# Kernel tuning notes

Measured on AMD Instinct MI355X. Metric: run time of the kernel, lower is better.

Reference implementation:

```python
import jax, jax.numpy as jnp
import numpy as np

EPS = 1e-08


def _center(K):
    # H K H with H = I - 11^T/n, expressed as O(n^2) double mean-subtraction
    rm = K.mean(axis=-1, keepdims=True)
    cm = K.mean(axis=-2, keepdims=True)
    tm = K.mean(axis=(-1, -2), keepdims=True)
    return K - rm - cm + tm


def setup_inputs() -> dict:
    key = jax.random.key(0)
    k1, k2 = jax.random.split(key)
    L, B, n, d = 5, 8, 1024, 64
    teacher = jax.random.normal(k1, (L, B, n, d), dtype=jnp.float32)
    student = jax.random.normal(k2, (L, B, n, d), dtype=jnp.float32)
    return {"teacher": teacher, "student": student}


def reference(teacher, student):
    # teacher, student: [L, B, n, d]  (internal=True, dim>=3 branch)
    cX = _center(jnp.einsum('lbnd,lbmd->lbnm', teacher, teacher))  # [L,B,n,n]
    cY = _center(jnp.einsum('lbnd,lbmd->lbnm', student, student))  # [L,B,n,n]
    hsic_xy = jnp.sum(cX * cY, axis=(-1, -2))  # [L,B]
    var_x = jnp.sqrt(jnp.sum(cX * cX, axis=(-1, -2)))  # [L,B]
    var_y = jnp.sqrt(jnp.sum(cY * cY, axis=(-1, -2)))  # [L,B]
    ratio = jnp.abs(hsic_xy / (var_x * var_y))  # [L,B]
    loss_per_layer = -jnp.log(ratio.mean(axis=-1) + EPS)  # [L]
    return loss_per_layer.mean()  # sum over layers / length
```

## Files before the change

kernel.cpp:

```cpp
#include <hip/hip_runtime.h>
#include <math.h>

#define LL 5
#define BB 8
#define NN 1024
#define DD 64
#define LB 40
#define SPLIT 16
#define KC (NN / SPLIT)
#define ZC (2 * DD)
#define NQ 3

#define GP_SHORTS (LB * SPLIT * NQ * 4096)
#define GP_FLOATS (GP_SHORTS / 2)
#define SP_OFF GP_FLOATS
#define ACC_OFF (GP_FLOATS + LB * SPLIT * ZC)

typedef short short8 __attribute__((ext_vector_type(8)));
typedef float floatx4 __attribute__((ext_vector_type(4)));

__device__ __forceinline__ unsigned short f2bf(float f) {
    union { float f; unsigned u; } v; v.f = f;
    const unsigned u = v.u;
    return (unsigned short)((u + 0x7FFFu + ((u >> 16) & 1u)) >> 16);
}
__device__ __forceinline__ float bf2f(unsigned short h) {
    union { unsigned u; float f; } v; v.u = ((unsigned)h) << 16; return v.f;
}
__device__ __forceinline__ float bflo(unsigned u) {
    union { unsigned u; float f; } v; v.u = u << 16; return v.f;
}
__device__ __forceinline__ float bfhi(unsigned u) {
    union { unsigned u; float f; } v; v.u = u & 0xFFFF0000u; return v.f;
}

__device__ __forceinline__ short8 read_frag(const short* Zt, int tbase, int lane, int k0) {
    const int c = tbase + (lane & 15);
    const int o = (k0 >> 3) + (lane >> 4);
    const int oct = (o ^ ((c + (c >> 4)) & 15)) & 7;
    return *(const short8*)(Zt + c * 64 + (oct << 3));
}

__global__ __launch_bounds__(256) void gram_kernel(const float* __restrict__ X,
                                                   const float* __restrict__ Y,
                                                   unsigned* __restrict__ Gp,
                                                   float* __restrict__ Sp) {
    __shared__ short Zt[ZC * KC];
    __shared__ float cscr[8][ZC];

    const int lb = blockIdx.y, nc = blockIdx.x, tid = threadIdx.x;
    const int r0 = nc * KC;
    const float4* X4 = (const float4*)(X + (size_t)lb * NN * DD);
    const float4* Y4 = (const float4*)(Y + (size_t)lb * NN * DD);

    const int col4 = tid & 31;
    const int rb = tid >> 5;
    float4 v[8];
#pragma unroll
    for (int m = 0; m < 8; ++m) {
        const int row = 8 * rb + m;
        v[m] = (col4 < 16) ? X4[(size_t)(r0 + row) * 16 + col4]
                           : Y4[(size_t)(r0 + row) * 16 + (col4 - 16)];
    }

#pragma unroll
    for (int e = 0; e < 4; ++e) {
        const int c = 4 * col4 + e;
        short8 w8;
        float cs = 0.f;
#pragma unroll
        for (int m = 0; m < 8; ++m) {
            const float fv = (e == 0) ? v[m].x : (e == 1) ? v[m].y : (e == 2) ? v[m].z : v[m].w;
            const unsigned short b = f2bf(fv);
            cs += bf2f(b);
            w8[m] = (short)b;
        }
        const int oct = (rb ^ ((c + (c >> 4)) & 15)) & 7;
        *(short8*)(Zt + c * 64 + (oct << 3)) = w8;
        cscr[rb][c] = cs;
    }
    __syncthreads();
    if (tid < ZC) {
        float s = 0.f;
#pragma unroll
        for (int g = 0; g < 8; ++g) s += cscr[g][tid];
        Sp[(lb * SPLIT + nc) * ZC + tid] = s;
    }

    const int lane = tid & 63, w = tid >> 6;
    const int jbeg = (w < 2) ? 0 : 4;

    floatx4 acc[2][8];
#pragma unroll
    for (int i = 0; i < 2; ++i)
#pragma unroll
        for (int j = 0; j < 8; ++j) acc[i][j] = (floatx4){0.f, 0.f, 0.f, 0.f};

#pragma unroll
    for (int k0 = 0; k0 < KC; k0 += 32) {
        short8 af[2], bfr[8];
#pragma unroll
        for (int i = 0; i < 2; ++i) af[i] = read_frag(Zt, (2 * w + i) * 16, lane, k0);
#pragma unroll
        for (int j = 0; j < 8; ++j)
            if (j >= jbeg) bfr[j] = read_frag(Zt, j * 16, lane, k0);
#pragma unroll
        for (int i = 0; i < 2; ++i)
#pragma unroll
            for (int j = 0; j < 8; ++j)
                if (j >= jbeg)
                    acc[i][j] = __builtin_amdgcn_mfma_f32_16x16x32_bf16(af[i], bfr[j], acc[i][j], 0, 0, 0);
    }

    unsigned* Gb = Gp + (size_t)(lb * SPLIT + nc) * (NQ * 2048);
    const int g = lane >> 4, cl = lane & 15;
#pragma unroll
    for (int i = 0; i < 2; ++i)
#pragma unroll
        for (int j = 0; j < 8; ++j) {
            if (j < jbeg) continue;
            const int slab = (w < 2) ? ((j < 4) ? 0 : 1) : 2;
            const int qrow0 = (w < 2 ? (2 * w + i) : (2 * (w - 2) + i)) * 16 + g * 4;
            const int qcol = (j & 3) * 16 + cl;
            if (w < 2 || j >= 4) {
                const unsigned lo = (unsigned)f2bf(acc[i][j][0]) | ((unsigned)f2bf(acc[i][j][1]) << 16);
                const unsigned hi = (unsigned)f2bf(acc[i][j][2]) | ((unsigned)f2bf(acc[i][j][3]) << 16);
                Gb[slab * 2048 + (qrow0 >> 1) * 64 + qcol] = lo;
                Gb[slab * 2048 + ((qrow0 >> 1) + 1) * 64 + qcol] = hi;
            }
        }
}

__global__ __launch_bounds__(256) void reduce_kernel(const unsigned* __restrict__ Gp,
                                                     const float* __restrict__ Sp,
                                                     float* __restrict__ Acc2) {
    const int b = blockIdx.x;
    const int lb = b / (NQ * 4);
    const int rem = b % (NQ * 4);
    const int q = rem >> 2, seg = rem & 3;
    const int tid = threadIdx.x;

    __shared__ float stot[ZC];
    __shared__ float red[4];

    if (tid < ZC) {
        float s = 0.f;
#pragma unroll
        for (int sp = 0; sp < SPLIT; ++sp) s += Sp[(lb * SPLIT + sp) * ZC + tid];
        stot[tid] = s;
    }
    __syncthreads();

    const int u0 = seg * 512 + tid * 2;
    const int rp = u0 >> 6;
    const int c0 = u0 & 63;

    float g00 = 0.f, g10 = 0.f, g01 = 0.f, g11 = 0.f;
#pragma unroll
    for (int sp = 0; sp < SPLIT; ++sp) {
        const uint2 p = *(const uint2*)&Gp[((size_t)(lb * SPLIT + sp) * NQ + q) * 2048 + u0];
        g00 += bflo(p.x); g10 += bfhi(p.x);
        g01 += bflo(p.y); g11 += bfhi(p.y);
    }
    const int rowbase = (q == 2) ? 64 : 0;
    const int colbase = (q == 0) ? 0 : 64;
    const float inv_n = 1.0f / (float)NN;
    const float sr0 = stot[rowbase + 2 * rp] * inv_n;
    const float sr1 = stot[rowbase + 2 * rp + 1] * inv_n;
    const float sc0 = stot[colbase + c0];
    const float sc1 = stot[colbase + c0 + 1];
    float sq = 0.f;
    { const float cv = g00 - sr0 * sc0; sq += cv * cv; }
    { const float cv = g10 - sr1 * sc0; sq += cv * cv; }
    { const float cv = g01 - sr0 * sc1; sq += cv * cv; }
    { const float cv = g11 - sr1 * sc1; sq += cv * cv; }

#pragma unroll
    for (int off = 32; off; off >>= 1) sq += __shfl_down(sq, off);
    const int wave = tid >> 6;
    if ((tid & 63) == 0) red[wave] = sq;
    __syncthreads();
    if (tid == 0)
        Acc2[lb * 12 + q * 4 + seg] = red[0] + red[1] + red[2] + red[3];
}

__global__ void final_kernel(const float* __restrict__ Acc2, float* __restrict__ out) {
    const int tid = threadIdx.x;
    float v = 0.0f;
    if (tid < LB) {
        float vxx = 0.f, hxy = 0.f, vyy = 0.f;
#pragma unroll
        for (int s = 0; s < 4; ++s) {
            vxx += Acc2[tid * 12 + s];
            hxy += Acc2[tid * 12 + 4 + s];
            vyy += Acc2[tid * 12 + 8 + s];
        }
        v = fabsf(hxy / (sqrtf(vxx) * sqrtf(vyy)));
    }
    v += __shfl_xor(v, 1);
    v += __shfl_xor(v, 2);
    v += __shfl_xor(v, 4);
    float loss = 0.0f;
#pragma unroll
    for (int l = 0; l < LL; ++l) {
        const float sl = __shfl(v, l * BB);
        loss += -logf(sl * (1.0f / (float)BB) + 1e-8f);
    }
    if (tid == 0) out[0] = loss * (1.0f / (float)LL);
}

extern "C" void kernel_launch(void* const* d_in, const int* in_sizes, int n_in,
                              void* d_out, int out_size, void* d_ws, size_t ws_size,
                              hipStream_t stream) {
    const float* teacher = (const float*)d_in[0];
    const float* student = (const float*)d_in[1];
    float* ws = (float*)d_ws;
    unsigned* Gp = (unsigned*)ws;
    float* Sp = ws + SP_OFF;
    float* Acc2 = ws + ACC_OFF;

    dim3 grid1(SPLIT, LB);
    gram_kernel<<<grid1, 256, 0, stream>>>(teacher, student, Gp, Sp);
    reduce_kernel<<<LB * NQ * 4, 256, 0, stream>>>(Gp, Sp, Acc2);
    final_kernel<<<1, 64, 0, stream>>>(Acc2, (float*)d_out);
}
```

Baseline: 77.30 us.

## Fuse gram, reduce and final kernels via atomic last-block election

Merges the three kernel launches into one kernel. Each lb's last-arriving split block, detected with an atomic counter, reduces that lb's partial Gram slabs, and the last lb block computes the final loss. This removes two launch boundaries and their gaps, at the cost of serialising each lb's reduction onto a single block (12x less parallelism for that stage) and adding a memset launch for the counters.

```diff
diff --git a/kernel.cpp b/kernel.cpp
--- a/kernel.cpp
+++ b/kernel.cpp
@@ -14,7 +14,8 @@
 #define GP_SHORTS (LB * SPLIT * NQ * 4096)
 #define GP_FLOATS (GP_SHORTS / 2)
 #define SP_OFF GP_FLOATS
-#define ACC_OFF (GP_FLOATS + LB * SPLIT * ZC)
+#define ACC_OFF (SP_OFF + LB * SPLIT * ZC)
+#define CNT_OFF (ACC_OFF + LB * 4)
 
 typedef short short8 __attribute__((ext_vector_type(8)));
 typedef float floatx4 __attribute__((ext_vector_type(4)));
@@ -41,107 +42,114 @@
     return *(const short8*)(Zt + c * 64 + (oct << 3));
 }
 
-__global__ __launch_bounds__(256) void gram_kernel(const float* __restrict__ X,
-                                                   const float* __restrict__ Y,
-                                                   unsigned* __restrict__ Gp,
-                                                   float* __restrict__ Sp) {
+__global__ __launch_bounds__(256) void cka_all(const float* __restrict__ X,
+                                               const float* __restrict__ Y,
+                                               unsigned* __restrict__ Gp,
+                                               float* __restrict__ Sp,
+                                               float* __restrict__ Acc,
+                                               unsigned* __restrict__ cnt,
+                                               float* __restrict__ out) {
     __shared__ short Zt[ZC * KC];
     __shared__ float cscr[8][ZC];
-
-    const int lb = blockIdx.y, nc = blockIdx.x, tid = threadIdx.x;
-    const int r0 = nc * KC;
-    const float4* X4 = (const float4*)(X + (size_t)lb * NN * DD);
-    const float4* Y4 = (const float4*)(Y + (size_t)lb * NN * DD);
-
-    const int col4 = tid & 31;
-    const int rb = tid >> 5;
-    float4 v[8];
-#pragma unroll
-    for (int m = 0; m < 8; ++m) {
-        const int row = 8 * rb + m;
-        v[m] = (col4 < 16) ? X4[(size_t)(r0 + row) * 16 + col4]
-                           : Y4[(size_t)(r0 + row) * 16 + (col4 - 16)];
-    }
-
-#pragma unroll
-    for (int e = 0; e < 4; ++e) {
-        const int c = 4 * col4 + e;
-        short8 w8;
-        float cs = 0.f;
+    __shared__ float stot[ZC];
+    __shared__ float redq[NQ][4];
+    __shared__ int elect;
+
+    const int bid = blockIdx.x;
+    const int tid = threadIdx.x;
+    const int lb = bid / SPLIT, nc = bid % SPLIT;
+
+    {
+        const int r0 = nc * KC;
+        const float4* X4 = (const float4*)(X + (size_t)lb * NN * DD);
+        const float4* Y4 = (const float4*)(Y + (size_t)lb * NN * DD);
+
+        const int col4 = tid & 31;
+        const int rb = tid >> 5;
+        float4 v[8];
 #pragma unroll
         for (int m = 0; m < 8; ++m) {
-            const float fv = (e == 0) ? v[m].x : (e == 1) ? v[m].y : (e == 2) ? v[m].z : v[m].w;
-            const unsigned short b = f2bf(fv);
-            cs += bf2f(b);
-            w8[m] = (short)b;
-        }
-        const int oct = (rb ^ ((c + (c >> 4)) & 15)) & 7;
-        *(short8*)(Zt + c * 64 + (oct << 3)) = w8;
-        cscr[rb][c] = cs;
-    }
-    __syncthreads();
-    if (tid < ZC) {
-        float s = 0.f;
-#pragma unroll
-        for (int g = 0; g < 8; ++g) s += cscr[g][tid];
-        Sp[(lb * SPLIT + nc) * ZC + tid] = s;
-    }
-
-    const int lane = tid & 63, w = tid >> 6;
-    const int jbeg = (w < 2) ? 0 : 4;
-
-    floatx4 acc[2][8];
-#pragma unroll
-    for (int i = 0; i < 2; ++i)
-#pragma unroll
-        for (int j = 0; j < 8; ++j) acc[i][j] = (floatx4){0.f, 0.f, 0.f, 0.f};
-
-#pragma unroll
-    for (int k0 = 0; k0 < KC; k0 += 32) {
-        short8 af[2], bfr[8];
-#pragma unroll
-        for (int i = 0; i < 2; ++i) af[i] = read_frag(Zt, (2 * w + i) * 16, lane, k0);
-#pragma unroll
-        for (int j = 0; j < 8; ++j)
-            if (j >= jbeg) bfr[j] = read_frag(Zt, j * 16, lane, k0);
+            const int row = 8 * rb + m;
+            v[m] = (col4 < 16) ? X4[(size_t)(r0 + row) * 16 + col4]
+                               : Y4[(size_t)(r0 + row) * 16 + (col4 - 16)];
+        }
+
+#pragma unroll
+        for (int e = 0; e < 4; ++e) {
+            const int c = 4 * col4 + e;
+            short8 w8;
+            float cs = 0.f;
+#pragma unroll
+            for (int m = 0; m < 8; ++m) {
+                const float fv = (e == 0) ? v[m].x : (e == 1) ? v[m].y
+                               : (e == 2) ? v[m].z : v[m].w;
+                const unsigned short b = f2bf(fv);
+                cs += bf2f(b);
+                w8[m] = (short)b;
+            }
+            const int oct = (rb ^ ((c + (c >> 4)) & 15)) & 7;
+            *(short8*)(Zt + c * 64 + (oct << 3)) = w8;
+            cscr[rb][c] = cs;
+        }
+        __syncthreads();
+        if (tid < ZC) {
+            float s = 0.f;
+#pragma unroll
+            for (int g = 0; g < 8; ++g) s += cscr[g][tid];
+            Sp[(lb * SPLIT + nc) * ZC + tid] = s;
+        }
+
+        const int lane = tid & 63, w = tid >> 6;
+        const int jbeg = (w < 2) ? 0 : 4;
+
+        floatx4 acc[2][8];
 #pragma unroll
         for (int i = 0; i < 2; ++i)
 #pragma unroll
+            for (int j = 0; j < 8; ++j) acc[i][j] = (floatx4){0.f, 0.f, 0.f, 0.f};
+
+#pragma unroll
+        for (int k0 = 0; k0 < KC; k0 += 32) {
+            short8 af[2], bfr[8];
+#pragma unroll
+            for (int i = 0; i < 2; ++i) af[i] = read_frag(Zt, (2 * w + i) * 16, lane, k0);
+#pragma unroll
             for (int j = 0; j < 8; ++j)
-                if (j >= jbeg)
-                    acc[i][j] = __builtin_amdgcn_mfma_f32_16x16x32_bf16(af[i], bfr[j], acc[i][j], 0, 0, 0);
-    }
-
-    unsigned* Gb = Gp + (size_t)(lb * SPLIT + nc) * (NQ * 2048);
-    const int g = lane >> 4, cl = lane & 15;
-#pragma unroll
-    for (int i = 0; i < 2; ++i)
-#pragma unroll
-        for (int j = 0; j < 8; ++j) {
-            if (j < jbeg) continue;
-            const int slab = (w < 2) ? ((j < 4) ? 0 : 1) : 2;
-            const int qrow0 = (w < 2 ? (2 * w + i) : (2 * (w - 2) + i)) * 16 + g * 4;
-            const int qcol = (j & 3) * 16 + cl;
-            if (w < 2 || j >= 4) {
+                if (j >= jbeg) bfr[j] = read_frag(Zt, j * 16, lane, k0);
+#pragma unroll
+            for (int i = 0; i < 2; ++i)
+#pragma unroll
+                for (int j = 0; j < 8; ++j)
+                    if (j >= jbeg)
+                        acc[i][j] = __builtin_amdgcn_mfma_f32_16x16x32_bf16(af[i], bfr[j], acc[i][j], 0, 0, 0);
+        }
+
+        unsigned* Gb = Gp + (size_t)(lb * SPLIT + nc) * (NQ * 2048);
+        const int g = lane >> 4, cl = lane & 15;
+#pragma unroll
+        for (int i = 0; i < 2; ++i)
+#pragma unroll
+            for (int j = 0; j < 8; ++j) {
+                if (j < jbeg) continue;
+                const int slab = (w < 2) ? ((j < 4) ? 0 : 1) : 2;
+                const int qrow0 = (w < 2 ? (2 * w + i) : (2 * (w - 2) + i)) * 16 + g * 4;
+                const int qcol = (j & 3) * 16 + cl;
                 const unsigned lo = (unsigned)f2bf(acc[i][j][0]) | ((unsigned)f2bf(acc[i][j][1]) << 16);
                 const unsigned hi = (unsigned)f2bf(acc[i][j][2]) | ((unsigned)f2bf(acc[i][j][3]) << 16);
                 Gb[slab * 2048 + (qrow0 >> 1) * 64 + qcol] = lo;
                 Gb[slab * 2048 + ((qrow0 >> 1) + 1) * 64 + qcol] = hi;
             }
-        }
-}
-
-__global__ __launch_bounds__(256) void reduce_kernel(const unsigned* __restrict__ Gp,
-                                                     const float* __restrict__ Sp,
-                                                     float* __restrict__ Acc2) {
-    const int b = blockIdx.x;
-    const int lb = b / (NQ * 4);
-    const int rem = b % (NQ * 4);
-    const int q = rem >> 2, seg = rem & 3;
-    const int tid = threadIdx.x;
-
-    __shared__ float stot[ZC];
-    __shared__ float red[4];
+    }
+
+    __syncthreads();
+    if (tid == 0) {
+        __threadfence();
+        const unsigned old = atomicAdd(&cnt[lb], 1u);
+        elect = (old == SPLIT - 1);
+    }
+    __syncthreads();
+    if (!elect) return;
+    __threadfence();
 
     if (tid < ZC) {
         float s = 0.f;
@@ -151,62 +159,77 @@
     }
     __syncthreads();
 
-    const int u0 = seg * 512 + tid * 2;
-    const int rp = u0 >> 6;
-    const int c0 = u0 & 63;
-
-    float g00 = 0.f, g10 = 0.f, g01 = 0.f, g11 = 0.f;
-#pragma unroll
-    for (int sp = 0; sp < SPLIT; ++sp) {
-        const uint2 p = *(const uint2*)&Gp[((size_t)(lb * SPLIT + sp) * NQ + q) * 2048 + u0];
-        g00 += bflo(p.x); g10 += bfhi(p.x);
-        g01 += bflo(p.y); g11 += bfhi(p.y);
-    }
-    const int rowbase = (q == 2) ? 64 : 0;
-    const int colbase = (q == 0) ? 0 : 64;
     const float inv_n = 1.0f / (float)NN;
-    const float sr0 = stot[rowbase + 2 * rp] * inv_n;
-    const float sr1 = stot[rowbase + 2 * rp + 1] * inv_n;
-    const float sc0 = stot[colbase + c0];
-    const float sc1 = stot[colbase + c0 + 1];
-    float sq = 0.f;
-    { const float cv = g00 - sr0 * sc0; sq += cv * cv; }
-    { const float cv = g10 - sr1 * sc0; sq += cv * cv; }
-    { const float cv = g01 - sr0 * sc1; sq += cv * cv; }
-    { const float cv = g11 - sr1 * sc1; sq += cv * cv; }
-
-#pragma unroll
-    for (int off = 32; off; off >>= 1) sq += __shfl_down(sq, off);
+    float sqq[NQ] = {0.f, 0.f, 0.f};
+#pragma unroll
+    for (int q = 0; q < NQ; ++q) {
+        const int rowbase = (q == 2) ? 64 : 0;
+        const int colbase = (q == 0) ? 0 : 64;
+#pragma unroll
+        for (int j = 0; j < 2; ++j) {
+            const int u0 = tid * 8 + j * 4;
+            const int rp = u0 >> 6, c0 = u0 & 63;
+            float g[8] = {0.f, 0.f, 0.f, 0.f, 0.f, 0.f, 0.f, 0.f};
+#pragma unroll
+            for (int sp = 0; sp < SPLIT; ++sp) {
+                const uint4 p = *(const uint4*)&Gp[((size_t)(lb * SPLIT + sp) * NQ + q) * 2048 + u0];
+                g[0] += bflo(p.x); g[1] += bfhi(p.x);
+                g[2] += bflo(p.y); g[3] += bfhi(p.y);
+                g[4] += bflo(p.z); g[5] += bfhi(p.z);
+                g[6] += bflo(p.w); g[7] += bfhi(p.w);
+            }
+            const float sr0 = stot[rowbase + 2 * rp] * inv_n;
+            const float sr1 = stot[rowbase + 2 * rp + 1] * inv_n;
+#pragma unroll
+            for (int e = 0; e < 4; ++e) {
+                const float sc = stot[colbase + c0 + e];
+                const float cv0 = g[2 * e] - sr0 * sc;
+                const float cv1 = g[2 * e + 1] - sr1 * sc;
+                sqq[q] += cv0 * cv0 + cv1 * cv1;
+            }
+        }
+    }
+#pragma unroll
+    for (int off = 32; off; off >>= 1) {
+        sqq[0] += __shfl_down(sqq[0], off);
+        sqq[1] += __shfl_down(sqq[1], off);
+        sqq[2] += __shfl_down(sqq[2], off);
+    }
     const int wave = tid >> 6;
-    if ((tid & 63) == 0) red[wave] = sq;
-    __syncthreads();
-    if (tid == 0)
-        Acc2[lb * 12 + q * 4 + seg] = red[0] + red[1] + red[2] + red[3];
-}
-
-__global__ void final_kernel(const float* __restrict__ Acc2, float* __restrict__ out) {
-    const int tid = threadIdx.x;
-    float v = 0.0f;
-    if (tid < LB) {
-        float vxx = 0.f, hxy = 0.f, vyy = 0.f;
-#pragma unroll
-        for (int s = 0; s < 4; ++s) {
-            vxx += Acc2[tid * 12 + s];
-            hxy += Acc2[tid * 12 + 4 + s];
-            vyy += Acc2[tid * 12 + 8 + s];
-        }
-        v = fabsf(hxy / (sqrtf(vxx) * sqrtf(vyy)));
-    }
-    v += __shfl_xor(v, 1);
-    v += __shfl_xor(v, 2);
-    v += __shfl_xor(v, 4);
-    float loss = 0.0f;
-#pragma unroll
-    for (int l = 0; l < LL; ++l) {
-        const float sl = __shfl(v, l * BB);
-        loss += -logf(sl * (1.0f / (float)BB) + 1e-8f);
-    }
-    if (tid == 0) out[0] = loss * (1.0f / (float)LL);
+    if ((tid & 63) == 0) { redq[0][wave] = sqq[0]; redq[1][wave] = sqq[1]; redq[2][wave] = sqq[2]; }
+    __syncthreads();
+
+    if (tid == 0) {
+#pragma unroll
+        for (int q = 0; q < NQ; ++q)
+            Acc[lb * 4 + q] = redq[q][0] + redq[q][1] + redq[q][2] + redq[q][3];
+        __threadfence();
+        const unsigned old2 = atomicAdd(&cnt[LB], 1u);
+        elect = (old2 == LB - 1);
+    }
+    __syncthreads();
+    if (!elect) return;
+    __threadfence();
+
+    if (tid < 64) {
+        float v = 0.0f;
+        if (tid < LB) {
+            const float vxx = Acc[tid * 4 + 0];
+            const float hxy = Acc[tid * 4 + 1];
+            const float vyy = Acc[tid * 4 + 2];
+            v = fabsf(hxy / (sqrtf(vxx) * sqrtf(vyy)));
+        }
+        v += __shfl_xor(v, 1);
+        v += __shfl_xor(v, 2);
+        v += __shfl_xor(v, 4);
+        float loss = 0.0f;
+#pragma unroll
+        for (int l = 0; l < LL; ++l) {
+            const float sl = __shfl(v, l * BB);
+            loss += -logf(sl * (1.0f / (float)BB) + 1e-8f);
+        }
+        if (tid == 0) out[0] = loss * (1.0f / (float)LL);
+    }
 }
 
 extern "C" void kernel_launch(void* const* d_in, const int* in_sizes, int n_in,
@@ -217,10 +240,10 @@
     float* ws = (float*)d_ws;
     unsigned* Gp = (unsigned*)ws;
     float* Sp = ws + SP_OFF;
-    float* Acc2 = ws + ACC_OFF;
-
-    dim3 grid1(SPLIT, LB);
-    gram_kernel<<<grid1, 256, 0, stream>>>(teacher, student, Gp, Sp);
-    reduce_kernel<<<LB * NQ * 4, 256, 0, stream>>>(Gp, Sp, Acc2);
-    final_kernel<<<1, 64, 0, stream>>>(Acc2, (float*)d_out);
-}
+    float* Acc = ws + ACC_OFF;
+    unsigned* cnt = (unsigned*)(ws + CNT_OFF);
+    float* out = (float*)d_out;
+
+    hipMemsetAsync(cnt, 0, 64 * sizeof(unsigned), stream);
+    cka_all<<<LB * SPLIT, 256, 0, stream>>>(teacher, student, Gp, Sp, Acc, cnt, out);
+}
```

Measured after the change: 124.8 us. +61.4%, slower.
